# Kernel optimization log

Hardware: AMD Instinct MI355X
Metric: run time of the kernel (lower is better)

## Reference

```python
import jax, jax.numpy as jnp
import numpy as np

INPUT_SIZE = 64
HIDDEN = 128
BATCH = 512
SEQ = 512


def setup_inputs() -> dict:
    key = jax.random.key(0)
    ks = jax.random.split(key, 7)
    s_ih = 1.0 / np.sqrt(HIDDEN)
    token = jax.random.normal(ks[0], (BATCH, SEQ, INPUT_SIZE), dtype=jnp.float32)
    W_ih = jax.random.uniform(ks[1], (HIDDEN, INPUT_SIZE), jnp.float32, -s_ih, s_ih)
    W_hh = jax.random.uniform(ks[2], (HIDDEN, HIDDEN), jnp.float32, -s_ih, s_ih)
    b_ih = jax.random.uniform(ks[3], (HIDDEN,), jnp.float32, -s_ih, s_ih)
    b_hh = jax.random.uniform(ks[4], (HIDDEN,), jnp.float32, -s_ih, s_ih)
    W_lin = jax.random.uniform(ks[5], (1, HIDDEN), jnp.float32, -s_ih, s_ih)
    b_lin = jax.random.uniform(ks[6], (1,), jnp.float32, -s_ih, s_ih)
    return {"token": token, "W_ih": W_ih, "W_hh": W_hh, "b_ih": b_ih,
            "b_hh": b_hh, "W_lin": W_lin, "b_lin": b_lin}


def reference(token, W_ih, W_hh, b_ih, b_hh, W_lin, b_lin):
    # Precompute input projection for all timesteps: [T, B, H]
    x_proj = jnp.einsum('bti,hi->tbh', token, W_ih) + b_ih + b_hh
    h0 = jnp.zeros((token.shape[0], W_hh.shape[0]), dtype=token.dtype)

    def step(h, xp):
        h_new = jnp.tanh(xp + h @ W_hh.T)
        return h_new, None

    h_last, _ = jax.lax.scan(step, h0, x_proj)
    # Linear head on last hidden state: [B, 1]
    return h_last @ W_lin.T + b_lin
```

## Files before the change

### kernel.cpp

```cpp
#include <hip/hip_runtime.h>

#define B_ 512
#define T_ 512
#define I_ 64
#define H_ 128
#define CHUNK 64
#define NCHUNK (T_ / CHUNK)

typedef float4 f4;

__device__ __forceinline__ float fast_tanh(float x) {
    float e = __expf(2.0f * x);
    return 1.0f - 2.0f * __builtin_amdgcn_rcpf(e + 1.0f);
}

template <int CTRL>
__device__ __forceinline__ float dppq(float x) {
    return __int_as_float(__builtin_amdgcn_update_dpp(
        0, __float_as_int(x), CTRL, 0xF, 0xF, true));
}

__device__ __forceinline__ void gload_lds16(const float* g, float* l) {
    __builtin_amdgcn_global_load_lds(
        (const __attribute__((address_space(1))) unsigned int*)g,
        (__attribute__((address_space(3))) unsigned int*)l, 16, 0, 0);
}

#define FMA4(A, X, W)                      \
    A.x = fmaf((X).x, (W).x, A.x);         \
    A.y = fmaf((X).y, (W).y, A.y);         \
    A.z = fmaf((X).z, (W).z, A.z);         \
    A.w = fmaf((X).w, (W).w, A.w);

__global__ __launch_bounds__(256) __attribute__((amdgpu_waves_per_eu(2, 2)))
void rnn_kernel(const float* __restrict__ token,
                const float* __restrict__ W_ih,
                const float* __restrict__ W_hh,
                const float* __restrict__ b_ih,
                const float* __restrict__ b_hh,
                const float* __restrict__ W_lin,
                const float* __restrict__ b_lin,
                float* __restrict__ out)
{
    __shared__ f4 tok_l[2][CHUNK * 16];
    __shared__ f4 h_l[2][32];

    const int tid = threadIdx.x;
    const int w   = tid >> 6;
    const int l   = tid & 63;
    const int q   = l & 3;
    const int Q   = (w << 4) | (l >> 2);
    const int b   = blockIdx.x;

    f4 wh0[8], wh1[8], wi0[4], wi1[4];
    {
        const f4* r0 = (const f4*)(W_hh + (2 * Q) * H_ + q * 32);
        const f4* r1 = (const f4*)(W_hh + (2 * Q + 1) * H_ + q * 32);
#pragma unroll
        for (int m = 0; m < 8; ++m) { wh0[m] = r0[m]; wh1[m] = r1[m]; }
        const f4* i0 = (const f4*)(W_ih + (2 * Q) * I_ + q * 16);
        const f4* i1 = (const f4*)(W_ih + (2 * Q + 1) * I_ + q * 16);
#pragma unroll
        for (int m = 0; m < 4; ++m) { wi0[m] = i0[m]; wi1[m] = i1[m]; }
    }
    const int   jsel    = 2 * Q + (q & 1);
    const float my_bias = b_ih[jsel] + b_hh[jsel];
    const int   wloc    = ((jsel >> 2) & 7) * 16 + (jsel >> 5) * 4 + (jsel & 3);
    const bool  writer  = (q < 2);

    const float* tok_row = token + (size_t)b * T_ * I_;

#pragma unroll
    for (int it = 0; it < 4; ++it) {
        const int S = it * 256 + tid;
        const int tt = S >> 4, k = S & 15, m = k >> 2, qk = k & 3;
        gload_lds16(tok_row + tt * 64 + qk * 16 + m * 4, (float*)&tok_l[0][S]);
    }
    if (tid < H_) ((float*)h_l[0])[tid] = 0.0f;
    asm volatile("s_waitcnt vmcnt(0) lgkmcnt(0)" ::: "memory");
    __builtin_amdgcn_s_barrier();

    f4 t4[4];
#pragma unroll
    for (int m = 0; m < 4; ++m) t4[m] = tok_l[0][m * 4 + q];

    auto STEP = [&](const f4* hrd, float* hwr, int tt, bool last_in_chunk,
                    bool has_next_chunk, int cb) {
        f4 A0 = {0.f, 0.f, 0.f, 0.f}, A1 = {0.f, 0.f, 0.f, 0.f};
#pragma unroll
        for (int m = 0; m < 4; ++m) { FMA4(A0, t4[m], wi0[m]); FMA4(A1, t4[m], wi1[m]); }
#pragma unroll
        for (int m = 0; m < 8; ++m) {
            f4 hv = hrd[m * 4 + q];
            FMA4(A0, hv, wh0[m]);
            FMA4(A1, hv, wh1[m]);
        }
        float p0 = (A0.x + A0.y) + (A0.z + A0.w);
        float p1 = (A1.x + A1.y) + (A1.z + A1.w);
        p0 += dppq<0xB1>(p0);  p1 += dppq<0xB1>(p1);
        p0 += dppq<0x4E>(p0);  p1 += dppq<0x4E>(p1);
        float hn = fast_tanh(((q & 1) ? p1 : p0) + my_bias);
        if (writer) hwr[wloc] = hn;

        if (!last_in_chunk) {
            __builtin_amdgcn_sched_barrier(0);
#pragma unroll
            for (int m = 0; m < 4; ++m) t4[m] = tok_l[cb][(tt + 1) * 16 + m * 4 + q];
            __builtin_amdgcn_sched_barrier(0);
            asm volatile("s_waitcnt lgkmcnt(4)" ::: "memory");
            __builtin_amdgcn_s_barrier();
        } else {
            asm volatile("s_waitcnt vmcnt(0) lgkmcnt(0)" ::: "memory");
            __builtin_amdgcn_s_barrier();
            if (has_next_chunk) {
#pragma unroll
                for (int m = 0; m < 4; ++m) t4[m] = tok_l[cb ^ 1][m * 4 + q];
            }
        }
    };

#pragma unroll 1
    for (int c = 0; c < NCHUNK; ++c) {
        const int cb = c & 1;
        const bool has_next = (c + 1 < NCHUNK);
        if (has_next) {
            const float* g = tok_row + (size_t)(c + 1) * CHUNK * I_;
#pragma unroll
            for (int it = 0; it < 4; ++it) {
                const int S = it * 256 + tid;
                const int tt = S >> 4, k = S & 15, m = k >> 2, qk = k & 3;
                gload_lds16(g + tt * 64 + qk * 16 + m * 4, (float*)&tok_l[cb ^ 1][S]);
            }
        }
#pragma unroll 1
        for (int tt = 0; tt < CHUNK; tt += 2) {
            STEP((const f4*)h_l[0], (float*)h_l[1], tt, false, has_next, cb);
            STEP((const f4*)h_l[1], (float*)h_l[0], tt + 1, (tt + 1 == CHUNK - 1),
                 has_next, cb);
        }
    }

    if (tid < 64) {
        const int j0 = tid, j1 = tid + 64;
        const int l0 = ((j0 >> 2) & 7) * 16 + (j0 >> 5) * 4 + (j0 & 3);
        const int l1 = ((j1 >> 2) & 7) * 16 + (j1 >> 5) * 4 + (j1 & 3);
        float p = ((const float*)h_l[0])[l0] * W_lin[j0]
                + ((const float*)h_l[0])[l1] * W_lin[j1];
#pragma unroll
        for (int off = 32; off; off >>= 1) p += __shfl_down(p, off);
        if (tid == 0) out[b] = p + b_lin[0];
    }
}

extern "C" void kernel_launch(void* const* d_in, const int* in_sizes, int n_in,
                              void* d_out, int out_size, void* d_ws, size_t ws_size,
                              hipStream_t stream) {
    const float* token = (const float*)d_in[0];
    const float* W_ih  = (const float*)d_in[1];
    const float* W_hh  = (const float*)d_in[2];
    const float* b_ih  = (const float*)d_in[3];
    const float* b_hh  = (const float*)d_in[4];
    const float* W_lin = (const float*)d_in[5];
    const float* b_lin = (const float*)d_in[6];
    float* out = (float*)d_out;

    hipLaunchKernelGGL(rnn_kernel, dim3(B_), dim3(256), 0, stream,
                       token, W_ih, W_hh, b_ih, b_hh, W_lin, b_lin, out);
}
```

Before: 241.4 us.

## Split each hidden-unit pair across 8 lanes with 512-thread blocks

Doubles the block to 512 threads so each pair of hidden units is computed by 8 lanes instead of 4. Each lane now holds half as many weight registers and does half the FMAs per step. The reduction gains extra row-level DPP steps, and the LDS layouts for h and tokens are remapped to match. This shortens the per-step serial dependency chain, at the cost of more waves taking part in each per-step barrier and more DPP reduction work.

```diff
diff --git a/kernel.cpp b/kernel.cpp
--- a/kernel.cpp
+++ b/kernel.cpp
@@ -14,10 +14,10 @@
     return 1.0f - 2.0f * __builtin_amdgcn_rcpf(e + 1.0f);
 }
 
-template <int CTRL>
-__device__ __forceinline__ float dppq(float x) {
+template <int CTRL, int BANK>
+__device__ __forceinline__ float dppf(float x) {
     return __int_as_float(__builtin_amdgcn_update_dpp(
-        0, __float_as_int(x), CTRL, 0xF, 0xF, true));
+        0, __float_as_int(x), CTRL, 0xF, BANK, true));
 }
 
 __device__ __forceinline__ void gload_lds16(const float* g, float* l) {
@@ -32,7 +32,9 @@
     A.z = fmaf((X).z, (W).z, A.z);         \
     A.w = fmaf((X).w, (W).w, A.w);
 
-__global__ __launch_bounds__(256) __attribute__((amdgpu_waves_per_eu(2, 2)))
+#define PIN4(v) asm volatile("" : "+v"((v).x), "+v"((v).y), "+v"((v).z), "+v"((v).w))
+
+__global__ __launch_bounds__(512) __attribute__((amdgpu_waves_per_eu(4, 4)))
 void rnn_kernel(const float* __restrict__ token,
                 const float* __restrict__ W_ih,
                 const float* __restrict__ W_hh,
@@ -46,75 +48,82 @@
     __shared__ f4 h_l[2][32];
 
     const int tid = threadIdx.x;
-    const int w   = tid >> 6;
     const int l   = tid & 63;
-    const int q   = l & 3;
-    const int Q   = (w << 4) | (l >> 2);
+    const int e   = l & 7;
+    const int G   = tid >> 3;
     const int b   = blockIdx.x;
 
-    f4 wh0[8], wh1[8], wi0[4], wi1[4];
+    f4 wh0[4], wh1[4], wi0[2], wi1[2];
     {
-        const f4* r0 = (const f4*)(W_hh + (2 * Q) * H_ + q * 32);
-        const f4* r1 = (const f4*)(W_hh + (2 * Q + 1) * H_ + q * 32);
+        const f4* r0 = (const f4*)(W_hh + (2 * G) * H_ + e * 16);
+        const f4* r1 = (const f4*)(W_hh + (2 * G + 1) * H_ + e * 16);
 #pragma unroll
-        for (int m = 0; m < 8; ++m) { wh0[m] = r0[m]; wh1[m] = r1[m]; }
-        const f4* i0 = (const f4*)(W_ih + (2 * Q) * I_ + q * 16);
-        const f4* i1 = (const f4*)(W_ih + (2 * Q + 1) * I_ + q * 16);
+        for (int m = 0; m < 4; ++m) { wh0[m] = r0[m]; wh1[m] = r1[m]; }
+        const f4* i0 = (const f4*)(W_ih + (2 * G) * I_ + e * 8);
+        const f4* i1 = (const f4*)(W_ih + (2 * G + 1) * I_ + e * 8);
 #pragma unroll
-        for (int m = 0; m < 4; ++m) { wi0[m] = i0[m]; wi1[m] = i1[m]; }
+        for (int m = 0; m < 2; ++m) { wi0[m] = i0[m]; wi1[m] = i1[m]; }
+#pragma unroll
+        for (int m = 0; m < 4; ++m) { PIN4(wh0[m]); PIN4(wh1[m]); }
+        PIN4(wi0[0]); PIN4(wi0[1]); PIN4(wi1[0]); PIN4(wi1[1]);
     }
-    const int   jsel    = 2 * Q + (q & 1);
+    const int   jsel    = 2 * G + (e & 1);
     const float my_bias = b_ih[jsel] + b_hh[jsel];
-    const int   wloc    = ((jsel >> 2) & 7) * 16 + (jsel >> 5) * 4 + (jsel & 3);
-    const bool  writer  = (q < 2);
+    const int   wloc    = ((jsel >> 2) & 3) * 32 + (jsel >> 4) * 4 + (jsel & 3);
+    const bool  writer  = (e < 2);
 
     const float* tok_row = token + (size_t)b * T_ * I_;
 
 #pragma unroll
-    for (int it = 0; it < 4; ++it) {
-        const int S = it * 256 + tid;
-        const int tt = S >> 4, k = S & 15, m = k >> 2, qk = k & 3;
-        gload_lds16(tok_row + tt * 64 + qk * 16 + m * 4, (float*)&tok_l[0][S]);
+    for (int it = 0; it < 2; ++it) {
+        const int S = it * 512 + tid;
+        const int tt = S >> 4, k = S & 15, m2 = k >> 3, ek = k & 7;
+        gload_lds16(tok_row + tt * 64 + ek * 8 + m2 * 4, (float*)&tok_l[0][S]);
     }
     if (tid < H_) ((float*)h_l[0])[tid] = 0.0f;
     asm volatile("s_waitcnt vmcnt(0) lgkmcnt(0)" ::: "memory");
     __builtin_amdgcn_s_barrier();
 
-    f4 t4[4];
-#pragma unroll
-    for (int m = 0; m < 4; ++m) t4[m] = tok_l[0][m * 4 + q];
+    f4 t4[2];
+    t4[0] = tok_l[0][e];
+    t4[1] = tok_l[0][8 + e];
 
     auto STEP = [&](const f4* hrd, float* hwr, int tt, bool last_in_chunk,
                     bool has_next_chunk, int cb) {
         f4 A0 = {0.f, 0.f, 0.f, 0.f}, A1 = {0.f, 0.f, 0.f, 0.f};
+        FMA4(A0, t4[0], wi0[0]);  FMA4(A1, t4[0], wi1[0]);
+        FMA4(A0, t4[1], wi0[1]);  FMA4(A1, t4[1], wi1[1]);
 #pragma unroll
-        for (int m = 0; m < 4; ++m) { FMA4(A0, t4[m], wi0[m]); FMA4(A1, t4[m], wi1[m]); }
-#pragma unroll
-        for (int m = 0; m < 8; ++m) {
-            f4 hv = hrd[m * 4 + q];
+        for (int m = 0; m < 4; ++m) {
+            f4 hv = hrd[m * 8 + e];
             FMA4(A0, hv, wh0[m]);
             FMA4(A1, hv, wh1[m]);
         }
         float p0 = (A0.x + A0.y) + (A0.z + A0.w);
         float p1 = (A1.x + A1.y) + (A1.z + A1.w);
-        p0 += dppq<0xB1>(p0);  p1 += dppq<0xB1>(p1);
-        p0 += dppq<0x4E>(p0);  p1 += dppq<0x4E>(p1);
-        float hn = fast_tanh(((q & 1) ? p1 : p0) + my_bias);
+        p0 += dppf<0xB1, 0xF>(p0);
+        p1 += dppf<0xB1, 0xF>(p1);
+        float c = (e & 1) ? p1 : p0;
+        c += dppf<0x4E, 0xF>(c);
+        float d1 = dppf<0x104, 0x5>(c);
+        float d2 = dppf<0x114, 0xA>(c);
+        c = c + d1 + d2;
+        float hn = fast_tanh(c + my_bias);
         if (writer) hwr[wloc] = hn;
 
         if (!last_in_chunk) {
             __builtin_amdgcn_sched_barrier(0);
-#pragma unroll
-            for (int m = 0; m < 4; ++m) t4[m] = tok_l[cb][(tt + 1) * 16 + m * 4 + q];
+            t4[0] = tok_l[cb][(tt + 1) * 16 + e];
+            t4[1] = tok_l[cb][(tt + 1) * 16 + 8 + e];
             __builtin_amdgcn_sched_barrier(0);
-            asm volatile("s_waitcnt lgkmcnt(4)" ::: "memory");
+            asm volatile("s_waitcnt lgkmcnt(2)" ::: "memory");
             __builtin_amdgcn_s_barrier();
         } else {
             asm volatile("s_waitcnt vmcnt(0) lgkmcnt(0)" ::: "memory");
             __builtin_amdgcn_s_barrier();
             if (has_next_chunk) {
-#pragma unroll
-                for (int m = 0; m < 4; ++m) t4[m] = tok_l[cb ^ 1][m * 4 + q];
+                t4[0] = tok_l[cb ^ 1][e];
+                t4[1] = tok_l[cb ^ 1][8 + e];
             }
         }
     };
@@ -126,10 +135,10 @@
         if (has_next) {
             const float* g = tok_row + (size_t)(c + 1) * CHUNK * I_;
 #pragma unroll
-            for (int it = 0; it < 4; ++it) {
-                const int S = it * 256 + tid;
-                const int tt = S >> 4, k = S & 15, m = k >> 2, qk = k & 3;
-                gload_lds16(g + tt * 64 + qk * 16 + m * 4, (float*)&tok_l[cb ^ 1][S]);
+            for (int it = 0; it < 2; ++it) {
+                const int S = it * 512 + tid;
+                const int tt = S >> 4, k = S & 15, m2 = k >> 3, ek = k & 7;
+                gload_lds16(g + tt * 64 + ek * 8 + m2 * 4, (float*)&tok_l[cb ^ 1][S]);
             }
         }
 #pragma unroll 1
@@ -142,8 +151,8 @@
 
     if (tid < 64) {
         const int j0 = tid, j1 = tid + 64;
-        const int l0 = ((j0 >> 2) & 7) * 16 + (j0 >> 5) * 4 + (j0 & 3);
-        const int l1 = ((j1 >> 2) & 7) * 16 + (j1 >> 5) * 4 + (j1 & 3);
+        const int l0 = ((j0 >> 2) & 3) * 32 + (j0 >> 4) * 4 + (j0 & 3);
+        const int l1 = ((j1 >> 2) & 3) * 32 + (j1 >> 4) * 4 + (j1 & 3);
         float p = ((const float*)h_l[0])[l0] * W_lin[j0]
                 + ((const float*)h_l[0])[l1] * W_lin[j1];
 #pragma unroll
@@ -164,6 +173,6 @@
     const float* b_lin = (const float*)d_in[6];
     float* out = (float*)d_out;
 
-    hipLaunchKernelGGL(rnn_kernel, dim3(B_), dim3(256), 0, stream,
+    hipLaunchKernelGGL(rnn_kernel, dim3(B_), dim3(512), 0, stream,
                        token, W_ih, W_hh, b_ih, b_hh, W_lin, b_lin, out);
 }
```

Result: faster. 234.3 us (-2.9%).
